# Kernel tuning notes

Measured on AMD Instinct MI355X. Metric: run time of the kernel, lower is better.

Reference implementation:

```python
import jax, jax.numpy as jnp
import numpy as np

N = 50000        # nodes
E = 800000       # edges (avg degree 16)
F_IN = 128       # in_features
F_OUT = 64       # out_features per head
HEADS = 4        # SparseGATConv default n_heads
ALPHA = 0.01     # LeakyReLU negative slope (SparseGATConv default alpha)


def setup_inputs() -> dict:
    key = jax.random.key(0)
    ks = jax.random.split(key, 6)
    x = jax.random.normal(ks[0], (N, F_IN), dtype=jnp.float32)
    edge_index = jax.random.randint(ks[1], (2, E), 0, N, dtype=jnp.int64)
    # xavier-normal-ish init, gain 1.414 as in the torch module
    W_heads = jax.random.normal(ks[2], (HEADS, F_IN, F_OUT), dtype=jnp.float32) * (1.414 / np.sqrt(F_IN))
    attn_heads = jax.random.normal(ks[3], (HEADS, 2 * F_OUT, 1), dtype=jnp.float32) * 0.1
    W_out = jax.random.normal(ks[4], (HEADS * F_OUT, F_OUT), dtype=jnp.float32) * (1.414 / np.sqrt(HEADS * F_OUT))
    attn_out = jax.random.normal(ks[5], (2 * F_OUT, 1), dtype=jnp.float32) * 0.1
    return {"x": x, "edge_index": edge_index, "W_heads": W_heads,
            "attn_heads": attn_heads, "W_out": W_out, "attn_out": attn_out}


def _sp_gat_layer(x, src, dst, W, attn, concat):
    """SpGraphAttentionLayer.forward: dense x @ W, edge attention scores,
    sparse row-softmax over COO adjacency, sparse-mm aggregation."""
    h = x @ W                                   # (N, d)
    d = h.shape[1]
    # cat(h[src], h[dst]) @ attn  ==  (h@a1)[src] + (h@a2)[dst]  (avoids (E,2d) concat)
    s1 = (h @ attn[:d]).squeeze(-1)             # (N,)
    s2 = (h @ attn[d:]).squeeze(-1)             # (N,)
    scores = -jax.nn.leaky_relu(s1[src] + s2[dst], negative_slope=ALPHA)  # (E,)
    # torch.sparse.softmax(dim=1): softmax over existing entries in each row (src)
    row_max = jax.ops.segment_max(scores, src, num_segments=N)
    ex = jnp.exp(scores - row_max[src])
    denom = jax.ops.segment_sum(ex, src, num_segments=N)
    a = ex / denom[src]                         # (E,) edge attention weights
    # sparse.mm: out[i] = sum_{e: src[e]=i} a[e] * h[dst[e]]
    out = jax.ops.segment_sum(a[:, None] * h[dst], src, num_segments=N)  # (N, d)
    return jax.nn.elu(out) if concat else out


def reference(x, edge_index, W_heads, attn_heads, W_out, attn_out):
    src, dst = edge_index[0], edge_index[1]
    # multi-head GAT layers (concat=True), then out_att on concatenated features
    heads_out = jax.vmap(lambda W, a: _sp_gat_layer(x, src, dst, W, a, True))(W_heads, attn_heads)  # (H, N, F_OUT)
    hcat = jnp.transpose(heads_out, (1, 0, 2)).reshape(N, HEADS * F_OUT)  # matches torch.cat(dim=1) head order
    return _sp_gat_layer(hcat, src, dst, W_out, attn_out, False)          # (N, F_OUT)
```

## Files before the change

kernel.cpp:

```cpp
#include <hip/hip_runtime.h>

typedef unsigned short u16;
typedef _Float16 f16;
typedef __attribute__((ext_vector_type(8))) _Float16 f16x8;
typedef __attribute__((ext_vector_type(2))) _Float16 f16x2;
typedef __attribute__((ext_vector_type(4))) float f32x4;

__device__ inline float nlrelu(float z) { return (z > 0.f) ? -z : -0.01f * z; }
__device__ inline float4 score4(float4 a, float4 b) {
    return make_float4(nlrelu(a.x + b.x), nlrelu(a.y + b.y), nlrelu(a.z + b.z), nlrelu(a.w + b.w));
}
__device__ inline unsigned packdup(float w) {
    f16x2 p = (f16x2){(f16)w, (f16)w};
    return __builtin_bit_cast(unsigned, p);
}

__global__ void k_init(const float* __restrict__ Wh, const float* __restrict__ Wo,
                       f16* __restrict__ B1, f16* __restrict__ B2,
                       int* __restrict__ counts, int* __restrict__ cursor, int N) {
    const int b = blockIdx.x;
    if (b < 128) {
        int i = b * 256 + threadIdx.x;
        int j = i & 7, lane = (i >> 3) & 63, kg = (i >> 9) & 3, nt = i >> 11;
        int n = nt * 16 + (lane & 15);
        int k = kg * 32 + ((lane >> 4) << 3) + j;
        B1[i] = (f16)Wh[(n >> 6) * (128 * 64) + k * 64 + (n & 63)];
    } else if (b < 192) {
        int i = (b - 128) * 256 + threadIdx.x;
        int j = i & 7, lane = (i >> 3) & 63, kg = (i >> 9) & 7, nt = i >> 12;
        int n = nt * 16 + (lane & 15);
        int k = kg * 32 + ((lane >> 4) << 3) + j;
        B2[i] = (f16)Wo[k * 64 + n];
    } else {
        int i = (b - 192) * 256 + threadIdx.x;
        if (i < N) { counts[i] = 0; cursor[i] = 0; }
    }
}

__global__ void count_edges(const int* __restrict__ src, int* __restrict__ counts, int E, int N) {
    int e = blockIdx.x * 256 + threadIdx.x;
    if (e >= E) return;
    int s = src[e];
    s = ((unsigned)s < (unsigned)N) ? s : 0;
    atomicAdd(&counts[s], 1);
}

__global__ __launch_bounds__(1024) void scan_p1(const int* __restrict__ counts, int* __restrict__ rowst,
                                                int* __restrict__ bsum, int n) {
    const int t = threadIdx.x, lane = t & 63, w = t >> 6;
    __shared__ int wsum[16];
    int i = blockIdx.x * 1024 + t;
    int v = (i < n) ? counts[i] : 0;
    int orig = v;
    for (int d = 1; d < 64; d <<= 1) { int x = __shfl_up(v, d); if (lane >= d) v += x; }
    if (lane == 63) wsum[w] = v;
    __syncthreads();
    if (t == 0) {
        int acc = 0;
        for (int j = 0; j < 16; j++) { int tmp = wsum[j]; wsum[j] = acc; acc += tmp; }
        bsum[blockIdx.x] = acc;
    }
    __syncthreads();
    if (i < n) rowst[i] = wsum[w] + (v - orig);
}

__global__ void scan_p3(const int* __restrict__ bsum, int* __restrict__ rowst, int n, int nb) {
    __shared__ int sh_pre, sh_tot;
    const int i = blockIdx.x * 256 + threadIdx.x;
    const int g = (blockIdx.x * 256) >> 10;
    if (threadIdx.x == 0) {
        int acc = 0, pre = 0;
        for (int j = 0; j < nb; j++) { if (j == g) pre = acc; acc += bsum[j]; }
        if (g >= nb) pre = acc;
        sh_pre = pre; sh_tot = acc;
    }
    __syncthreads();
    if (i < n) rowst[i] += sh_pre;
    else if (i == n) rowst[n] = sh_tot;
}

__global__ __launch_bounds__(256) void k_scatter_gemm1(
        const int* __restrict__ src, const int* __restrict__ dst,
        const int* __restrict__ rowst, int* __restrict__ cursor, int* __restrict__ edged,
        const float* __restrict__ X, const f16* __restrict__ B1, const float* __restrict__ attnH,
        f16* __restrict__ H1, float* __restrict__ s1, float* __restrict__ s2,
        int M, int E, int N, int Gg) {
    if ((int)blockIdx.x >= Gg) {
        int e = (blockIdx.x - Gg) * 256 + threadIdx.x;
        if (e >= E) return;
        int s = src[e];
        s = ((unsigned)s < (unsigned)N) ? s : 0;
        int d = dst[e];
        d = ((unsigned)d < (unsigned)N) ? d : 0;
        int pos = atomicAdd(&cursor[s], 1);
        edged[rowst[s] + pos] = d;
        return;
    }
    const int lane = threadIdx.x & 63, wave = threadIdx.x >> 6;
    const int row0 = (blockIdx.x * 4 + wave) * 16;
    if (row0 >= M) return;
    const int mrow = row0 + (lane & 15);
    const int koff = (lane >> 4) * 8;
    const float* aptr = X + (size_t)mrow * 128 + koff;

    f32x4 acc[16];
#pragma unroll
    for (int c = 0; c < 16; c++) acc[c] = (f32x4){0.f, 0.f, 0.f, 0.f};

#pragma unroll
    for (int kg = 0; kg < 4; kg++) {
        float av[8];
        *(float4*)av       = *(const float4*)(aptr + kg * 32);
        *(float4*)(av + 4) = *(const float4*)(aptr + kg * 32 + 4);
        f16x8 a;
#pragma unroll
        for (int j = 0; j < 8; j++) a[j] = (f16)av[j];
#pragma unroll
        for (int nt = 0; nt < 16; nt++) {
            const size_t bidx = (size_t)(((nt << 2) + kg) * 64 + lane) * 8;
            f16x8 bfr = *(const f16x8*)(B1 + bidx);
            acc[nt] = __builtin_amdgcn_mfma_f32_16x16x32_f16(a, bfr, acc[nt], 0, 0, 0);
        }
    }
    const int rbase = (lane >> 4) * 4;
    const int colq = lane & 15;
#pragma unroll
    for (int h = 0; h < 4; h++) {
        float s1a[4] = {0.f, 0.f, 0.f, 0.f}, s2a[4] = {0.f, 0.f, 0.f, 0.f};
#pragma unroll
        for (int q = 0; q < 4; q++) {
            const int nt = h * 4 + q;
            const int col = nt * 16 + colq;
            const float a1v = attnH[h * 128 + (col & 63)];
            const float a2v = attnH[h * 128 + 64 + (col & 63)];
#pragma unroll
            for (int r = 0; r < 4; r++) {
                float c = acc[nt][r];
                H1[(size_t)(row0 + rbase + r) * 256 + col] = (f16)c;
                s1a[r] += c * a1v;
                s2a[r] += c * a2v;
            }
        }
#pragma unroll
        for (int off = 1; off < 16; off <<= 1)
#pragma unroll
            for (int r = 0; r < 4; r++) {
                s1a[r] += __shfl_xor(s1a[r], off);
                s2a[r] += __shfl_xor(s2a[r], off);
            }
        if (colq == 0)
#pragma unroll
            for (int r = 0; r < 4; r++) {
                s1[(size_t)(row0 + rbase + r) * 4 + h] = s1a[r];
                s2[(size_t)(row0 + rbase + r) * 4 + h] = s2a[r];
            }
    }
}

__global__ __launch_bounds__(256) void gemm2_f16(const f16* __restrict__ Hc, const f16* __restrict__ B2,
        const float* __restrict__ attnO,
        f16* __restrict__ H2, float* __restrict__ s1b, float* __restrict__ s2b, int M) {
    const int lane = threadIdx.x & 63, wave = threadIdx.x >> 6;
    const int row0 = (blockIdx.x * 4 + wave) * 16;
    if (row0 >= M) return;
    const int mrow = row0 + (lane & 15);
    const int koff = (lane >> 4) * 8;
    const f16* ap = Hc + (size_t)mrow * 256 + koff;

    f32x4 acc[4];
#pragma unroll
    for (int c = 0; c < 4; c++) acc[c] = (f32x4){0.f, 0.f, 0.f, 0.f};

#pragma unroll
    for (int kg = 0; kg < 8; kg++) {
        f16x8 a = *(const f16x8*)(ap + kg * 32);
#pragma unroll
        for (int nt = 0; nt < 4; nt++) {
            const size_t bidx = (size_t)(((nt << 3) + kg) * 64 + lane) * 8;
            f16x8 bfr = *(const f16x8*)(B2 + bidx);
            acc[nt] = __builtin_amdgcn_mfma_f32_16x16x32_f16(a, bfr, acc[nt], 0, 0, 0);
        }
    }
    const int rbase = (lane >> 4) * 4;
    const int colq = lane & 15;
    float s1a[4] = {0.f, 0.f, 0.f, 0.f}, s2a[4] = {0.f, 0.f, 0.f, 0.f};
#pragma unroll
    for (int nt = 0; nt < 4; nt++) {
        const int col = nt * 16 + colq;
        const float a1v = attnO[col];
        const float a2v = attnO[64 + col];
#pragma unroll
        for (int r = 0; r < 4; r++) {
            float c = acc[nt][r];
            H2[(size_t)(row0 + rbase + r) * 64 + col] = (f16)c;
            s1a[r] += c * a1v;
            s2a[r] += c * a2v;
        }
    }
#pragma unroll
    for (int off = 1; off < 16; off <<= 1)
#pragma unroll
        for (int r = 0; r < 4; r++) {
            s1a[r] += __shfl_xor(s1a[r], off);
            s2a[r] += __shfl_xor(s2a[r], off);
        }
    if (colq == 0)
#pragma unroll
        for (int r = 0; r < 4; r++) {
            s1b[row0 + rbase + r] = s1a[r];
            s2b[row0 + rbase + r] = s2a[r];
        }
}

__global__ __launch_bounds__(256) void agg_l1(const int* __restrict__ rowst, const int* __restrict__ edged,
                                              const float* __restrict__ s1, const float* __restrict__ s2,
                                              const f16* __restrict__ H, f16* __restrict__ hcat, int N) {
    __shared__ unsigned wls[4][64][4];
    __shared__ int dls[4][64];
    const int t = threadIdx.x, lane = t & 63, wave = t >> 6;
    const int node = blockIdx.x * 4 + wave;
    if (node >= N) return;
    const int beg = rowst[node], end = rowst[node + 1];
    const int deg = end - beg;
    const int head = lane >> 4;
    f16* outp = hcat + (size_t)node * 256 + lane * 4;
    if (deg == 0) { *(uint2*)outp = make_uint2(0u, 0u); return; }
    const float4 s1v = *(const float4*)(s1 + (size_t)node * 4);

    float r0, r1, r2, r3;
    if (deg <= 64) {
        int d = 0;
        if (lane < deg) d = edged[beg + lane];
        dls[wave][lane] = d;
        float4 s2v = *(const float4*)(s2 + (size_t)d * 4);
        float4 sc = score4(s1v, s2v);
        if (lane >= deg) sc = make_float4(-3e38f, -3e38f, -3e38f, -3e38f);
        float4 m = sc;
#pragma unroll
        for (int off = 32; off > 0; off >>= 1) {
            m.x = fmaxf(m.x, __shfl_xor(m.x, off));
            m.y = fmaxf(m.y, __shfl_xor(m.y, off));
            m.z = fmaxf(m.z, __shfl_xor(m.z, off));
            m.w = fmaxf(m.w, __shfl_xor(m.w, off));
        }
        float4 ex = make_float4(0.f, 0.f, 0.f, 0.f);
        if (lane < deg) ex = make_float4(__expf(sc.x - m.x), __expf(sc.y - m.y),
                                         __expf(sc.z - m.z), __expf(sc.w - m.w));
        float4 sm = ex;
#pragma unroll
        for (int off = 32; off > 0; off >>= 1) {
            sm.x += __shfl_xor(sm.x, off);
            sm.y += __shfl_xor(sm.y, off);
            sm.z += __shfl_xor(sm.z, off);
            sm.w += __shfl_xor(sm.w, off);
        }
        wls[wave][lane][0] = packdup(ex.x / sm.x);
        wls[wave][lane][1] = packdup(ex.y / sm.y);
        wls[wave][lane][2] = packdup(ex.z / sm.z);
        wls[wave][lane][3] = packdup(ex.w / sm.w);
        f16x2 a01[4], a23[4];
#pragma unroll
        for (int j = 0; j < 4; j++) { a01[j] = (f16x2)(f16)0.f; a23[j] = (f16x2)(f16)0.f; }
        int e = 0;
        for (; e + 4 <= deg; e += 4) {
#pragma unroll
            for (int j = 0; j < 4; j++) {
                int dd = dls[wave][e + j];
                uint2 raw = *(const uint2*)(H + (size_t)dd * 256 + lane * 4);
                f16x2 lo = __builtin_bit_cast(f16x2, raw.x);
                f16x2 hi = __builtin_bit_cast(f16x2, raw.y);
                f16x2 w2 = __builtin_bit_cast(f16x2, wls[wave][e + j][head]);
                a01[j] += w2 * lo;
                a23[j] += w2 * hi;
            }
        }
        for (; e < deg; e++) {
            int dd = dls[wave][e];
            uint2 raw = *(const uint2*)(H + (size_t)dd * 256 + lane * 4);
            f16x2 lo = __builtin_bit_cast(f16x2, raw.x);
            f16x2 hi = __builtin_bit_cast(f16x2, raw.y);
            f16x2 w2 = __builtin_bit_cast(f16x2, wls[wave][e][head]);
            a01[0] += w2 * lo;
            a23[0] += w2 * hi;
        }
        r0 = (float)a01[0][0] + (float)a01[1][0] + (float)a01[2][0] + (float)a01[3][0];
        r1 = (float)a01[0][1] + (float)a01[1][1] + (float)a01[2][1] + (float)a01[3][1];
        r2 = (float)a23[0][0] + (float)a23[1][0] + (float)a23[2][0] + (float)a23[3][0];
        r3 = (float)a23[0][1] + (float)a23[1][1] + (float)a23[2][1] + (float)a23[3][1];
    } else {
        float4 m = make_float4(-3e38f, -3e38f, -3e38f, -3e38f);
        for (int e = beg + lane; e < end; e += 64) {
            int d = edged[e];
            float4 sc = score4(s1v, *(const float4*)(s2 + (size_t)d * 4));
            m.x = fmaxf(m.x, sc.x); m.y = fmaxf(m.y, sc.y); m.z = fmaxf(m.z, sc.z); m.w = fmaxf(m.w, sc.w);
        }
#pragma unroll
        for (int off = 32; off > 0; off >>= 1) {
            m.x = fmaxf(m.x, __shfl_xor(m.x, off));
            m.y = fmaxf(m.y, __shfl_xor(m.y, off));
            m.z = fmaxf(m.z, __shfl_xor(m.z, off));
            m.w = fmaxf(m.w, __shfl_xor(m.w, off));
        }
        float4 sm = make_float4(0.f, 0.f, 0.f, 0.f);
        for (int e = beg + lane; e < end; e += 64) {
            int d = edged[e];
            float4 sc = score4(s1v, *(const float4*)(s2 + (size_t)d * 4));
            sm.x += __expf(sc.x - m.x); sm.y += __expf(sc.y - m.y);
            sm.z += __expf(sc.z - m.z); sm.w += __expf(sc.w - m.w);
        }
#pragma unroll
        for (int off = 32; off > 0; off >>= 1) {
            sm.x += __shfl_xor(sm.x, off);
            sm.y += __shfl_xor(sm.y, off);
            sm.z += __shfl_xor(sm.z, off);
            sm.w += __shfl_xor(sm.w, off);
        }
        float4 inv = make_float4(1.f / sm.x, 1.f / sm.y, 1.f / sm.z, 1.f / sm.w);
        float4 acc = make_float4(0.f, 0.f, 0.f, 0.f);
        for (int e = beg; e < end; e++) {
            int dd = edged[e];
            float4 sc = score4(s1v, *(const float4*)(s2 + (size_t)dd * 4));
            float wv[4] = { __expf(sc.x - m.x) * inv.x, __expf(sc.y - m.y) * inv.y,
                            __expf(sc.z - m.z) * inv.z, __expf(sc.w - m.w) * inv.w };
            float w = (head == 0) ? wv[0] : (head == 1) ? wv[1] : (head == 2) ? wv[2] : wv[3];
            const f16* hp = H + (size_t)dd * 256 + lane * 4;
            acc.x += w * (float)hp[0]; acc.y += w * (float)hp[1];
            acc.z += w * (float)hp[2]; acc.w += w * (float)hp[3];
        }
        r0 = acc.x; r1 = acc.y; r2 = acc.z; r3 = acc.w;
    }
    r0 = (r0 > 0.f) ? r0 : (__expf(r0) - 1.f);
    r1 = (r1 > 0.f) ? r1 : (__expf(r1) - 1.f);
    r2 = (r2 > 0.f) ? r2 : (__expf(r2) - 1.f);
    r3 = (r3 > 0.f) ? r3 : (__expf(r3) - 1.f);
    f16x2 o0 = (f16x2){(f16)r0, (f16)r1};
    f16x2 o1 = (f16x2){(f16)r2, (f16)r3};
    *(uint2*)outp = make_uint2(__builtin_bit_cast(unsigned, o0), __builtin_bit_cast(unsigned, o1));
}

__global__ __launch_bounds__(256) void agg_l2(const int* __restrict__ rowst, const int* __restrict__ edged,
                                              const float* __restrict__ s1, const float* __restrict__ s2,
                                              const f16* __restrict__ H, float* __restrict__ outp, int N) {
    __shared__ float wls[4][64];
    __shared__ int dls[4][64];
    const int t = threadIdx.x, lane = t & 63, wave = t >> 6;
    const int node = blockIdx.x * 4 + wave;
    if (node >= N) return;
    const int beg = rowst[node], end = rowst[node + 1];
    const int deg = end - beg;
    if (deg == 0) { outp[(size_t)node * 64 + lane] = 0.f; return; }
    const float s1v = s1[node];

    float acc = 0.f;
    if (deg <= 64) {
        int d = 0;
        if (lane < deg) d = edged[beg + lane];
        dls[wave][lane] = d;
        float z = s1v + s2[d];
        float sc = (lane < deg) ? nlrelu(z) : -3e38f;
        float m = sc;
#pragma unroll
        for (int off = 32; off > 0; off >>= 1) m = fmaxf(m, __shfl_xor(m, off));
        float ex = (lane < deg) ? __expf(sc - m) : 0.f;
        float sm = ex;
#pragma unroll
        for (int off = 32; off > 0; off >>= 1) sm += __shfl_xor(sm, off);
        wls[wave][lane] = ex / sm;
        int e = 0;
        for (; e + 4 <= deg; e += 4) {
            int d0 = dls[wave][e], d1 = dls[wave][e + 1], d2 = dls[wave][e + 2], d3 = dls[wave][e + 3];
            float h0 = (float)H[(size_t)d0 * 64 + lane];
            float h1 = (float)H[(size_t)d1 * 64 + lane];
            float h2 = (float)H[(size_t)d2 * 64 + lane];
            float h3 = (float)H[(size_t)d3 * 64 + lane];
            acc += wls[wave][e] * h0 + wls[wave][e + 1] * h1 + wls[wave][e + 2] * h2 + wls[wave][e + 3] * h3;
        }
        for (; e < deg; e++)
            acc += wls[wave][e] * (float)H[(size_t)dls[wave][e] * 64 + lane];
    } else {
        float m = -3e38f;
        for (int e = beg + lane; e < end; e += 64) {
            int d = edged[e];
            m = fmaxf(m, nlrelu(s1v + s2[d]));
        }
#pragma unroll
        for (int off = 32; off > 0; off >>= 1) m = fmaxf(m, __shfl_xor(m, off));
        float sm = 0.f;
        for (int e = beg + lane; e < end; e += 64) {
            int d = edged[e];
            sm += __expf(nlrelu(s1v + s2[d]) - m);
        }
#pragma unroll
        for (int off = 32; off > 0; off >>= 1) sm += __shfl_xor(sm, off);
        float inv = 1.f / sm;
        for (int e = beg; e < end; e++) {
            int dd = edged[e];
            float w = __expf(nlrelu(s1v + s2[dd]) - m) * inv;
            acc += w * (float)H[(size_t)dd * 64 + lane];
        }
    }
    outp[(size_t)node * 64 + lane] = acc;
}

extern "C" void kernel_launch(void* const* d_in, const int* in_sizes, int n_in,
                              void* d_out, int out_size, void* d_ws, size_t ws_size,
                              hipStream_t stream) {
    const float* x     = (const float*)d_in[0];
    const int*   ei    = (const int*)d_in[1];
    const float* Wh    = (const float*)d_in[2];
    const float* attnH = (const float*)d_in[3];
    const float* Wo    = (const float*)d_in[4];
    const float* attnO = (const float*)d_in[5];
    float* out         = (float*)d_out;

    const int N = in_sizes[0] / 128;
    const int E = in_sizes[1] / 2;
    const int* srcp = ei;
    const int* dstp = ei + E;

    char* base = (char*)d_ws;
    size_t off = 0;
    auto take = [&](size_t b) { void* p = base + off; off += (b + 255) & ~(size_t)255; return p; };
    f16*   B1     = (f16*)  take(32768 * 2);
    f16*   B2     = (f16*)  take(16384 * 2);
    int*   counts = (int*)  take((size_t)N * 4);
    int*   cursor = (int*)  take((size_t)N * 4);
    int*   rowst  = (int*)  take((size_t)(N + 1) * 4);
    int*   edged  = (int*)  take((size_t)E * 4);
    int*   bsum   = (int*)  take(4096);
    float* s1     = (float*)take((size_t)N * 4 * 4);
    float* s2     = (float*)take((size_t)N * 4 * 4);
    float* s1b    = (float*)take((size_t)N * 4);
    float* s2b    = (float*)take((size_t)N * 4);
    f16*   H1     = (f16*)  take((size_t)N * 256 * 2);
    f16*   hcat   = (f16*)  take((size_t)N * 256 * 2);
    f16*   H2     = (f16*)  take((size_t)N * 64 * 2);

    const int zb = (N + 255) / 256;
    k_init<<<192 + zb, 256, 0, stream>>>(Wh, Wo, B1, B2, counts, cursor, N);

    count_edges<<<(E + 255) / 256, 256, 0, stream>>>(srcp, counts, E, N);
    const int nb = (N + 1023) / 1024;
    scan_p1<<<nb, 1024, 0, stream>>>(counts, rowst, bsum, N);
    scan_p3<<<(N + 256) / 256, 256, 0, stream>>>(bsum, rowst, N, nb);

    const int Gg = (N + 63) / 64;
    const int Gs = (E + 255) / 256;
    k_scatter_gemm1<<<Gg + Gs, 256, 0, stream>>>(srcp, dstp, rowst, cursor, edged,
                                                 x, B1, attnH, H1, s1, s2, N, E, N, Gg);

    agg_l1<<<(N + 3) / 4, 256, 0, stream>>>(rowst, edged, s1, s2, H1, hcat, N);
    gemm2_f16<<<Gg, 256, 0, stream>>>(hcat, B2, attnO, H2, s1b, s2b, N);
    agg_l2<<<(N + 3) / 4, 256, 0, stream>>>(rowst, edged, s1b, s2b, H2, out, N);
}
```

Baseline: 276.6 us.

## Record edge slot during counting to drop second atomic pass in CSR build

The counting kernel now stores each edge's atomicAdd return value as its slot within the source row. Scatter then becomes a plain indexed write with no atomics, so the cursor array and its zeroing go away. The scatter is split out of the fused GEMM1 launch into its own kernel, and both edge kernels handle four edges per thread. In exchange it adds an E-sized pos buffer that must be written and read back, one extra launch, and it loses the overlap between scatter and GEMM1.

```diff
diff --git a/kernel.cpp b/kernel.cpp
--- a/kernel.cpp
+++ b/kernel.cpp
@@ -17,7 +17,7 @@
 
 __global__ void k_init(const float* __restrict__ Wh, const float* __restrict__ Wo,
                        f16* __restrict__ B1, f16* __restrict__ B2,
-                       int* __restrict__ counts, int* __restrict__ cursor, int N) {
+                       int* __restrict__ counts, int N) {
     const int b = blockIdx.x;
     if (b < 128) {
         int i = b * 256 + threadIdx.x;
@@ -33,16 +33,22 @@
         B2[i] = (f16)Wo[k * 64 + n];
     } else {
         int i = (b - 192) * 256 + threadIdx.x;
-        if (i < N) { counts[i] = 0; cursor[i] = 0; }
-    }
-}
-
-__global__ void count_edges(const int* __restrict__ src, int* __restrict__ counts, int E, int N) {
-    int e = blockIdx.x * 256 + threadIdx.x;
-    if (e >= E) return;
-    int s = src[e];
-    s = ((unsigned)s < (unsigned)N) ? s : 0;
-    atomicAdd(&counts[s], 1);
+        if (i < N) counts[i] = 0;
+    }
+}
+
+__global__ __launch_bounds__(256) void count_pos(const int* __restrict__ src, int* __restrict__ counts,
+                                                 int* __restrict__ pos, int E, int N) {
+    const int base = blockIdx.x * 1024 + threadIdx.x;
+#pragma unroll
+    for (int j = 0; j < 4; j++) {
+        int e = base + j * 256;
+        if (e < E) {
+            int s = src[e];
+            s = ((unsigned)s < (unsigned)N) ? s : 0;
+            pos[e] = atomicAdd(&counts[s], 1);
+        }
+    }
 }
 
 __global__ __launch_bounds__(1024) void scan_p1(const int* __restrict__ counts, int* __restrict__ rowst,
@@ -79,23 +85,26 @@
     else if (i == n) rowst[n] = sh_tot;
 }
 
-__global__ __launch_bounds__(256) void k_scatter_gemm1(
-        const int* __restrict__ src, const int* __restrict__ dst,
-        const int* __restrict__ rowst, int* __restrict__ cursor, int* __restrict__ edged,
-        const float* __restrict__ X, const f16* __restrict__ B1, const float* __restrict__ attnH,
-        f16* __restrict__ H1, float* __restrict__ s1, float* __restrict__ s2,
-        int M, int E, int N, int Gg) {
-    if ((int)blockIdx.x >= Gg) {
-        int e = (blockIdx.x - Gg) * 256 + threadIdx.x;
-        if (e >= E) return;
-        int s = src[e];
-        s = ((unsigned)s < (unsigned)N) ? s : 0;
-        int d = dst[e];
-        d = ((unsigned)d < (unsigned)N) ? d : 0;
-        int pos = atomicAdd(&cursor[s], 1);
-        edged[rowst[s] + pos] = d;
-        return;
-    }
+__global__ __launch_bounds__(256) void scatter_noat(const int* __restrict__ src, const int* __restrict__ dst,
+                                                    const int* __restrict__ rowst, const int* __restrict__ pos,
+                                                    int* __restrict__ edged, int E, int N) {
+    const int base = blockIdx.x * 1024 + threadIdx.x;
+#pragma unroll
+    for (int j = 0; j < 4; j++) {
+        int e = base + j * 256;
+        if (e < E) {
+            int s = src[e];
+            s = ((unsigned)s < (unsigned)N) ? s : 0;
+            int d = dst[e];
+            d = ((unsigned)d < (unsigned)N) ? d : 0;
+            edged[rowst[s] + pos[e]] = d;
+        }
+    }
+}
+
+__global__ __launch_bounds__(256) void gemm1_f16(const float* __restrict__ X, const f16* __restrict__ B1,
+        const float* __restrict__ attnH,
+        f16* __restrict__ H1, float* __restrict__ s1, float* __restrict__ s2, int M) {
     const int lane = threadIdx.x & 63, wave = threadIdx.x >> 6;
     const int row0 = (blockIdx.x * 4 + wave) * 16;
     if (row0 >= M) return;
@@ -424,8 +433,8 @@
     f16*   B1     = (f16*)  take(32768 * 2);
     f16*   B2     = (f16*)  take(16384 * 2);
     int*   counts = (int*)  take((size_t)N * 4);
-    int*   cursor = (int*)  take((size_t)N * 4);
     int*   rowst  = (int*)  take((size_t)(N + 1) * 4);
+    int*   pos    = (int*)  take((size_t)E * 4);
     int*   edged  = (int*)  take((size_t)E * 4);
     int*   bsum   = (int*)  take(4096);
     float* s1     = (float*)take((size_t)N * 4 * 4);
@@ -437,18 +446,19 @@
     f16*   H2     = (f16*)  take((size_t)N * 64 * 2);
 
     const int zb = (N + 255) / 256;
-    k_init<<<192 + zb, 256, 0, stream>>>(Wh, Wo, B1, B2, counts, cursor, N);
-
-    count_edges<<<(E + 255) / 256, 256, 0, stream>>>(srcp, counts, E, N);
+    k_init<<<192 + zb, 256, 0, stream>>>(Wh, Wo, B1, B2, counts, N);
+
+    const int eb4 = (E + 1023) / 1024;
+    count_pos<<<eb4, 256, 0, stream>>>(srcp, counts, pos, E, N);
+
     const int nb = (N + 1023) / 1024;
     scan_p1<<<nb, 1024, 0, stream>>>(counts, rowst, bsum, N);
     scan_p3<<<(N + 256) / 256, 256, 0, stream>>>(bsum, rowst, N, nb);
 
+    scatter_noat<<<eb4, 256, 0, stream>>>(srcp, dstp, rowst, pos, edged, E, N);
+
     const int Gg = (N + 63) / 64;
-    const int Gs = (E + 255) / 256;
-    k_scatter_gemm1<<<Gg + Gs, 256, 0, stream>>>(srcp, dstp, rowst, cursor, edged,
-                                                 x, B1, attnH, H1, s1, s2, N, E, N, Gg);
-
+    gemm1_f16<<<Gg, 256, 0, stream>>>(x, B1, attnH, H1, s1, s2, N);
     agg_l1<<<(N + 3) / 4, 256, 0, stream>>>(rowst, edged, s1, s2, H1, hcat, N);
     gemm2_f16<<<Gg, 256, 0, stream>>>(hcat, B2, attnO, H2, s1b, s2b, N);
     agg_l2<<<(N + 3) / 4, 256, 0, stream>>>(rowst, edged, s1b, s2b, H2, out, N);
```

After: 262.9 us. 5.0% less time.
